# Optimization experiments

Measured on AMD Instinct MI355X. Metric: run time of the kernel, lower is better.

## Reference

```python
import jax, jax.numpy as jnp
import numpy as np

B, L, E, H = 2, 2048, 1024, 16
D = E // H  # 64


def setup_inputs() -> dict:
    key = jax.random.key(0)
    ks = jax.random.split(key, 9)
    return {
        "query": jax.random.normal(ks[0], (B, L, E), dtype=jnp.float32),
        "value": jax.random.normal(ks[1], (B, L, E), dtype=jnp.float32),
        "key": jax.random.normal(ks[2], (B, L, E), dtype=jnp.float32),
        "mask": jax.random.randint(ks[3], (B, 1, L, L), 0, 2, dtype=jnp.int32),
        "Wq": jax.random.normal(ks[4], (D, D), dtype=jnp.float32) * 0.05,
        "Wk": jax.random.normal(ks[5], (D, D), dtype=jnp.float32) * 0.05,
        "Wv": jax.random.normal(ks[6], (D, D), dtype=jnp.float32) * 0.05,
        "Wfc": jax.random.normal(ks[7], (E, E), dtype=jnp.float32) * 0.02,
        "bfc": jax.random.normal(ks[8], (E,), dtype=jnp.float32) * 0.02,
    }


def reference(query, value, key, mask, Wq, Wk, Wv, Wfc, bfc):
    b, q_len, _ = query.shape
    k_len = key.shape[1]
    v_len = value.shape[1]
    # split heads: [b, l, H, D]
    q = query.reshape(b, q_len, H, D)
    k = key.reshape(b, k_len, H, D)
    v = value.reshape(b, v_len, H, D)
    # per-head linear projections (shared weights across heads, no bias)
    q = jnp.einsum('bqhd,ed->bqhe', q, Wq)
    k = jnp.einsum('bkhd,ed->bkhe', k, Wk)
    v = jnp.einsum('bvhd,ed->bvhe', v, Wv)
    # attention scores [b, H, q, k]
    attn = jnp.einsum('bqhd,bkhd->bhqk', q, k)
    # NOTE: original masks BEFORE scaling, and scales by sqrt(embedding_size)
    attn = jnp.where(mask == 0, jnp.float32(-1e20), attn)
    attn = attn / jnp.float32(E ** 0.5)
    attn = jax.nn.softmax(attn, axis=3)
    out = jnp.einsum('bhqk,bkhd->bqhd', attn, v).reshape(b, q_len, E)
    out = out @ Wfc.T + bfc
    return out
```

## Files before the change

kernel.cpp:

```cpp
#include <hip/hip_runtime.h>
#include <hip/hip_bf16.h>


#define B_ 2
#define L_ 2048
#define E_ 1024
#define H_ 16
#define D_ 64

typedef __attribute__((ext_vector_type(8))) short s8v;
typedef __attribute__((ext_vector_type(4))) float f4v;
typedef __attribute__((ext_vector_type(2))) float f2v;

__device__ __forceinline__ f4v mfma16(s8v a, s8v b, f4v c) {
    return __builtin_amdgcn_mfma_f32_16x16x32_bf16(a, b, c, 0, 0, 0);
}

__device__ __forceinline__ float fast_exp2(float x) {
    return __builtin_amdgcn_exp2f(x);
}

__device__ __forceinline__ ushort bf16bits(float f) {
    __hip_bfloat16 h = __float2bfloat16(f);
    return *(ushort*)&h;
}

__device__ __forceinline__ void glds16(const __hip_bfloat16* g, ushort* l) {
    __builtin_amdgcn_global_load_lds(
        (const __attribute__((address_space(1))) void*)g,
        (__attribute__((address_space(3))) void*)l,
        16, 0, 0);
}

__device__ __forceinline__ s8v ld8_dual(const void* p, size_t idx, bool isf32) {
    if (isf32) {
        const float* pf = (const float*)p + idx;
        f4v f0 = *(const f4v*)pf;
        f4v f1 = *(const f4v*)(pf + 4);
        s8v r;
        r[0] = (short)bf16bits(f0[0]); r[1] = (short)bf16bits(f0[1]);
        r[2] = (short)bf16bits(f0[2]); r[3] = (short)bf16bits(f0[3]);
        r[4] = (short)bf16bits(f1[0]); r[5] = (short)bf16bits(f1[1]);
        r[6] = (short)bf16bits(f1[2]); r[7] = (short)bf16bits(f1[3]);
        return r;
    }
    return *(const s8v*)((const __hip_bfloat16*)p + idx);
}

__device__ __forceinline__ s8v ld8_ws(const __hip_bfloat16* p) {
    return *(const s8v*)p;
}

__device__ __forceinline__ s8v u4_to_s8(uint a, uint b, uint c, uint d) {
    union { uint u[4]; s8v v; } x;
    x.u[0] = a; x.u[1] = b; x.u[2] = c; x.u[3] = d;
    return x.v;
}

__device__ __forceinline__ bool block_detect_f32(const void* q_in, int* sflag) {
    if (threadIdx.x == 0) *sflag = 0;
    __syncthreads();
    const ushort* qq = (const ushort*)q_in + (threadIdx.x & 255) * 16;
    int bad = 0;
    #pragma unroll
    for (int i = 0; i < 16; ++i) bad += (((qq[i] >> 7) & 0xFF) >= 0x8E);
    bad += __shfl_xor(bad, 1);
    bad += __shfl_xor(bad, 2);
    bad += __shfl_xor(bad, 4);
    bad += __shfl_xor(bad, 8);
    bad += __shfl_xor(bad, 16);
    bad += __shfl_xor(bad, 32);
    if ((threadIdx.x & 63) == 0 && threadIdx.x < 256) atomicAdd(sflag, bad);
    __syncthreads();
    return *sflag > 100;
}

__device__ __forceinline__ void cvt_piece(
    size_t i4, const void* Wfc, const void* bfc,
    __hip_bfloat16* wfc_bf, __hip_bfloat16* bfc_bf, bool isf32)
{
    const size_t base = i4 * 4;
    const size_t n1 = (size_t)E_ * E_;
    if (base >= n1 + E_) return;
    const void* src = (base < n1) ? Wfc : bfc;
    const size_t off = (base < n1) ? base : base - n1;
    __hip_bfloat16* dst = (base < n1) ? (wfc_bf + off) : (bfc_bf + off);
    if (isf32) {
        f4v v = *(const f4v*)((const float*)src + off);
        #pragma unroll
        for (int j = 0; j < 4; ++j) dst[j] = __float2bfloat16(v[j]);
    } else {
        *(ushort4*)dst = *(const ushort4*)((const ushort*)src + off);
    }
}

__global__ __launch_bounds__(256) void proj_all_kernel(
    const void* __restrict__ q_in, const void* __restrict__ k_in,
    const void* __restrict__ v_in,
    const void* __restrict__ Wq, const void* __restrict__ Wk,
    const void* __restrict__ Wv,
    const void* __restrict__ Wfc, const void* __restrict__ bfc,
    const int* __restrict__ mask, unsigned long long* __restrict__ mbits,
    __hip_bfloat16* __restrict__ qp, __hip_bfloat16* __restrict__ kp,
    __hip_bfloat16* __restrict__ vpT,
    __hip_bfloat16* __restrict__ wfc_bf, __hip_bfloat16* __restrict__ bfc_bf)
{
    __shared__ __align__(16) ushort tile[64][72];
    __shared__ __align__(16) ushort wlds[64 * 72];
    __shared__ int sflag;
    const int wave = threadIdx.x >> 6;
    const int lane = threadIdx.x & 63;
    const int quad = lane >> 4;
    const int l16  = lane & 15;

    if (blockIdx.y == 3) {
        const int lane_ = threadIdx.x & 63;
        const size_t wbase = (size_t)blockIdx.x * 128 + wave * 32;
        #pragma unroll 4
        for (int i = 0; i < 32; ++i) {
            const size_t widx = wbase + i;
            const int v = mask[widx * 64 + lane_];
            const unsigned long long bal = __ballot(v != 0);
            if (lane_ == 0) mbits[widx] = bal;
        }
        return;
    }

    const bool isf32 = block_detect_f32(q_in, &sflag);

    if (blockIdx.y == 4) {
        cvt_piece((size_t)blockIdx.x * 256 + threadIdx.x, Wfc, bfc, wfc_bf, bfc_bf, isf32);
        if (blockIdx.x == 0)
            cvt_piece((size_t)(E_ * (size_t)E_ / 4) + threadIdx.x, Wfc, bfc, wfc_bf, bfc_bf, isf32);
        return;
    }

    {
        const void* W = blockIdx.y == 0 ? Wq : (blockIdx.y == 1 ? Wk : Wv);
        const int row = threadIdx.x >> 2;
        const int c0  = (threadIdx.x & 3) * 16;
        if (isf32) {
            const float* wsrc = (const float*)W + row * 64 + c0;
            #pragma unroll
            for (int j = 0; j < 16; ++j)
                wlds[row * 72 + c0 + j] = bf16bits(wsrc[j]);
        } else {
            const ushort* wsrc = (const ushort*)W + row * 64 + c0;
            *(s8v*)&wlds[row * 72 + c0]     = *(const s8v*)wsrc;
            *(s8v*)&wlds[row * 72 + c0 + 8] = *(const s8v*)(wsrc + 8);
        }
    }
    __syncthreads();

    if (blockIdx.y < 2) {
        const void* X = blockIdx.y == 0 ? q_in : k_in;
        __hip_bfloat16* dst = blockIdx.y == 0 ? qp : kp;
        const float oscale = (blockIdx.y == 0) ? 0.045084439755930314f : 1.0f;
        const int m0 = (blockIdx.x * 4 + wave) * 16;

        const size_t abase = (size_t)(m0 + l16) * D_;
        s8v a0 = ld8_dual(X, abase + quad * 8, isf32);
        s8v a1 = ld8_dual(X, abase + 32 + quad * 8, isf32);

        f4v acc[4];
        #pragma unroll
        for (int nt = 0; nt < 4; ++nt) {
            const ushort* wr = &wlds[(nt * 16 + l16) * 72];
            s8v b0 = *(const s8v*)(wr + quad * 8);
            s8v b1 = *(const s8v*)(wr + 32 + quad * 8);
            f4v c = {0.f, 0.f, 0.f, 0.f};
            c = mfma16(a0, b0, c);
            c = mfma16(a1, b1, c);
            acc[nt] = c;
        }
        #pragma unroll
        for (int r = 0; r < 4; ++r) {
            const int m = m0 + quad * 4 + r;
            const int h = m & 15;
            const int bl = m >> 4;
            const int b = bl >> 11;
            const int l = bl & (L_ - 1);
            #pragma unroll
            for (int nt = 0; nt < 4; ++nt) {
                const int e = nt * 16 + l16;
                dst[(((size_t)(b * H_ + h)) * L_ + l) * D_ + e] =
                    __float2bfloat16(acc[nt][r] * oscale);
            }
        }
    } else {
        const int l0 = (blockIdx.x & 31) * 64;
        const int bh = blockIdx.x >> 5;
        const int b = bh >> 4, h = bh & 15;
        const int lw = l0 + wave * 16;

        const size_t xbase = ((size_t)(b * L_ + lw + l16)) * E_ + h * D_;
        s8v a0 = ld8_dual(v_in, xbase + quad * 8, isf32);
        s8v a1 = ld8_dual(v_in, xbase + 32 + quad * 8, isf32);

        #pragma unroll
        for (int nt = 0; nt < 4; ++nt) {
            const int e = nt * 16 + l16;
            const ushort* wr = &wlds[e * 72];
            s8v b0 = *(const s8v*)(wr + quad * 8);
            s8v b1 = *(const s8v*)(wr + 32 + quad * 8);
            f4v c = {0.f, 0.f, 0.f, 0.f};
            c = mfma16(a0, b0, c);
            c = mfma16(a1, b1, c);
            #pragma unroll
            for (int r = 0; r < 4; ++r)
                tile[wave * 16 + quad * 4 + r][e] = bf16bits(c[r]);
        }
        __syncthreads();
        const int e  = threadIdx.x >> 2;
        const int lc = (threadIdx.x & 3) * 16;
        s8v s0, s1;
        #pragma unroll
        for (int i = 0; i < 8; ++i) {
            s0[i] = (short)tile[lc + i][e];
            s1[i] = (short)tile[lc + 8 + i][e];
        }
        __hip_bfloat16* drow = vpT + ((size_t)bh * D_ + e) * L_ + l0 + lc;
        *(s8v*)drow = s0;
        *(s8v*)(drow + 8) = s1;
    }
}

__global__ __launch_bounds__(256) void cvt_wfc_kernel(
    const void* __restrict__ Wfc, const void* __restrict__ bfc,
    __hip_bfloat16* __restrict__ wfc_bf, __hip_bfloat16* __restrict__ bfc_bf,
    const void* __restrict__ q_in)
{
    __shared__ int sflag;
    const bool isf32 = block_detect_f32(q_in, &sflag);
    cvt_piece((size_t)blockIdx.x * 256 + threadIdx.x, Wfc, bfc, wfc_bf, bfc_bf, isf32);
}

__global__ __launch_bounds__(512, 2) void attn_kernel(
    const __hip_bfloat16* __restrict__ qp,
    const __hip_bfloat16* __restrict__ kp,
    const __hip_bfloat16* __restrict__ vpT,
    const unsigned long long* __restrict__ mbits,
    __hip_bfloat16* __restrict__ attn_out)
{
    __shared__ __align__(16) ushort kv[4][2][64 * 64];

    const int wave = threadIdx.x >> 6;
    const int lane = threadIdx.x & 63;
    const int quad = lane >> 4;
    const int l16  = lane & 15;
    const int sw   = l16 & 7;
    const int bh = blockIdx.y;
    const int b = bh >> 4, h = bh & 15;
    const int q0 = blockIdx.x * 128 + wave * 16;

    const __hip_bfloat16* kbh = kp + (size_t)bh * L_ * D_;
    const __hip_bfloat16* vbh = vpT + (size_t)bh * D_ * L_;
    const unsigned long long* mrow = mbits + ((size_t)b * L_ + q0 + l16) * 32;

    const int lrow = lane >> 3;
    const int lchk = (lane & 7) ^ lrow;
    const int r0 = wave * 8;
    const __hip_bfloat16* kg = kbh + (size_t)(r0 + lrow) * D_ + lchk * 8;
    const __hip_bfloat16* vg = vbh + (size_t)(r0 + lrow) * L_ + lchk * 8;

    const __hip_bfloat16* qbase = qp + ((size_t)bh * L_ + q0) * D_;
    s8v qa0 = ld8_ws(qbase + (size_t)l16 * D_ + quad * 8);
    s8v qa1 = ld8_ws(qbase + (size_t)l16 * D_ + 32 + quad * 8);

    f2v rs2 = {0.f, 0.f};
    f4v o[4];
    #pragma unroll
    for (int nt = 0; nt < 4; ++nt) o[nt] = (f4v){0.f, 0.f, 0.f, 0.f};

    const int ro0 = l16 * 64 + ((quad ^ sw) << 3);
    const int ro1 = l16 * 64 + (((quad + 4) ^ sw) << 3);
    const int shq = quad * 4;

    unsigned long long wq0 = 0, wq1 = 0, wq2 = 0, wq3 = 0;

    glds16(kg, &kv[0][0][r0 * 64]);
    glds16(vg, &kv[0][1][r0 * 64]);
    wq0 = mrow[0];
    kg += 64 * D_; vg += 64;
    glds16(kg, &kv[1][0][r0 * 64]);
    glds16(vg, &kv[1][1][r0 * 64]);
    wq1 = mrow[1];
    kg += 64 * D_; vg += 64;

#define ATTN_BODY(IT_, CUR_, DST_, PRE_, VMASM_)                               \
    {                                                                          \
        if (PRE_) {                                                            \
            glds16(kg, &kv[DST_][0][r0 * 64]);                                 \
            glds16(vg, &kv[DST_][1][r0 * 64]);                                 \
            wq##DST_ = mrow[(IT_) + 2];                                        \
            kg += 64 * D_; vg += 64;                                           \
        }                                                                      \
        asm volatile(VMASM_ ::: "memory");                                     \
        __builtin_amdgcn_s_barrier();                                          \
        __builtin_amdgcn_sched_barrier(0);                                     \
        const uint wlo_sh = ((uint)wq##CUR_) >> shq;                           \
        const uint whi_sh = ((uint)(wq##CUR_ >> 32)) >> shq;                   \
        f4v s_[4];                                                             \
        __builtin_amdgcn_s_setprio(1);                                         \
        _Pragma("unroll")                                                      \
        for (int nt = 0; nt < 4; ++nt) {                                       \
            s8v kb0 = *(const s8v*)&kv[CUR_][0][nt * 1024 + ro0];              \
            s8v kb1 = *(const s8v*)&kv[CUR_][0][nt * 1024 + ro1];              \
            f4v c = {0.f, 0.f, 0.f, 0.f};                                      \
            c = mfma16(kb0, qa0, c);                                           \
            c = mfma16(kb1, qa1, c);                                           \
            s_[nt] = c;                                                        \
        }                                                                      \
        __builtin_amdgcn_s_setprio(0);                                         \
        uint dw[4][2];                                                         \
        _Pragma("unroll")                                                      \
        for (int nt = 0; nt < 4; ++nt) {                                       \
            const uint hs = (nt & 2) ? whi_sh : wlo_sh;                        \
            float pr[4];                                                       \
            _Pragma("unroll")                                                  \
            for (int r = 0; r < 4; ++r) {                                      \
                const float p = fast_exp2(s_[nt][r]);                          \
                const int m = __builtin_amdgcn_sbfe((int)hs,                   \
                                  ((nt & 1) << 4) + r, 1);                     \
                pr[r] = __uint_as_float(__float_as_uint(p) & (uint)m);         \
            }                                                                  \
            rs2 += (f2v){pr[0], pr[1]};                                        \
            rs2 += (f2v){pr[2], pr[3]};                                        \
            asm("v_cvt_pk_bf16_f32 %0, %1, %2"                                 \
                : "=v"(dw[nt][0]) : "v"(pr[0]), "v"(pr[1]));                   \
            asm("v_cvt_pk_bf16_f32 %0, %1, %2"                                 \
                : "=v"(dw[nt][1]) : "v"(pr[2]), "v"(pr[3]));                   \
        }                                                                      \
        uint w00 = dw[0][0], w10 = dw[1][0];                                   \
        uint w01 = dw[0][1], w11 = dw[1][1];                                   \
        uint w20 = dw[2][0], w30 = dw[3][0];                                   \
        uint w21 = dw[2][1], w31 = dw[3][1];                                   \
        asm("v_permlane32_swap_b32 %0, %1" : "+v"(w00), "+v"(w10));            \
        asm("v_permlane16_swap_b32 %0, %1" : "+v"(w00), "+v"(w10));            \
        asm("v_permlane32_swap_b32 %0, %1" : "+v"(w01), "+v"(w11));            \
        asm("v_permlane16_swap_b32 %0, %1" : "+v"(w01), "+v"(w11));            \
        asm("v_permlane32_swap_b32 %0, %1" : "+v"(w20), "+v"(w30));            \
        asm("v_permlane16_swap_b32 %0, %1" : "+v"(w20), "+v"(w30));            \
        asm("v_permlane32_swap_b32 %0, %1" : "+v"(w21), "+v"(w31));            \
        asm("v_permlane16_swap_b32 %0, %1" : "+v"(w21), "+v"(w31));            \
        s8v pa0 = u4_to_s8(w00, w01, w10, w11);                                \
        s8v pa1 = u4_to_s8(w20, w21, w30, w31);                                \
        __builtin_amdgcn_s_setprio(1);                                         \
        _Pragma("unroll")                                                      \
        for (int nt = 0; nt < 4; ++nt) {                                       \
            s8v vb0 = *(const s8v*)&kv[CUR_][1][nt * 1024 + ro0];              \
            s8v vb1 = *(const s8v*)&kv[CUR_][1][nt * 1024 + ro1];              \
            o[nt] = mfma16(pa0, vb0, o[nt]);                                   \
            o[nt] = mfma16(pa1, vb1, o[nt]);                                   \
        }                                                                      \
        __builtin_amdgcn_s_setprio(0);                                         \
    }

    for (int it4 = 0; it4 < 7; ++it4) {
        const int t = it4 * 4;
        ATTN_BODY(t,     0, 2, true, "s_waitcnt vmcnt(6)")
        ATTN_BODY(t + 1, 1, 3, true, "s_waitcnt vmcnt(6)")
        ATTN_BODY(t + 2, 2, 0, true, "s_waitcnt vmcnt(6)")
        ATTN_BODY(t + 3, 3, 1, true, "s_waitcnt vmcnt(6)")
    }
    ATTN_BODY(28, 0, 2, true,  "s_waitcnt vmcnt(6)")
    ATTN_BODY(29, 1, 3, true,  "s_waitcnt vmcnt(6)")
    ATTN_BODY(30, 2, 0, false, "s_waitcnt vmcnt(3)")
    ATTN_BODY(31, 3, 1, false, "s_waitcnt vmcnt(0)")
#undef ATTN_BODY

    float v = rs2[0] + rs2[1];
    v += __shfl_xor(v, 16, 64);
    v += __shfl_xor(v, 32, 64);
    #pragma unroll
    for (int r = 0; r < 4; ++r) {
        const int qrow = quad * 4 + r;
        const float li = __shfl(v, qrow, 64);
        const float inv = 1.0f / fmaxf(li, 1e-30f);
        const int row = q0 + qrow;
        #pragma unroll
        for (int nt = 0; nt < 4; ++nt) {
            const int d = nt * 16 + l16;
            attn_out[((size_t)(b * L_ + row)) * E_ + h * D_ + d] =
                __float2bfloat16(o[nt][r] * inv);
        }
    }
}

__global__ __launch_bounds__(256, 4) void fc_kernel(
    const __hip_bfloat16* __restrict__ x,
    const __hip_bfloat16* __restrict__ wfc_bf,
    const __hip_bfloat16* __restrict__ bfc_bf,
    void* __restrict__ out, const void* __restrict__ q_in)
{
    __shared__ __align__(16) ushort abuf[2][128 * 64];
    __shared__ __align__(16) ushort bbuf[2][64 * 64];
    __shared__ int sflag;
    const bool isf32 = block_detect_f32(q_in, &sflag);
    const int wave = threadIdx.x >> 6;
    const int lane = threadIdx.x & 63;
    const int quad = lane >> 4;
    const int l16  = lane & 15;
    const int sw   = l16 & 7;
    const int m0 = blockIdx.x * 128;
    const int n0 = blockIdx.y * 64;
    const int wr = wave >> 1;
    const int wc = wave & 1;

    const int lrow = lane >> 3;
    const int lchk = (lane & 7) ^ lrow;

    const __hip_bfloat16* ag[4];
    #pragma unroll
    for (int c = 0; c < 4; ++c)
        ag[c] = x + (size_t)(m0 + c * 32 + wave * 8 + lrow) * E_ + lchk * 8;
    const __hip_bfloat16* bg[2];
    #pragma unroll
    for (int c = 0; c < 2; ++c)
        bg[c] = wfc_bf + (size_t)(n0 + c * 32 + wave * 8 + lrow) * E_ + lchk * 8;

    f4v acc[4][2];
    #pragma unroll
    for (int fm = 0; fm < 4; ++fm)
        #pragma unroll
        for (int fn = 0; fn < 2; ++fn) acc[fm][fn] = (f4v){0.f, 0.f, 0.f, 0.f};

    #pragma unroll
    for (int c = 0; c < 4; ++c) glds16(ag[c], &abuf[0][(c * 32 + wave * 8) * 64]);
    #pragma unroll
    for (int c = 0; c < 2; ++c) glds16(bg[c], &bbuf[0][(c * 32 + wave * 8) * 64]);
    __syncthreads();

    int cur = 0;
    for (int it = 0; it < 16; ++it) {
        if (it < 15) {
            #pragma unroll
            for (int c = 0; c < 4; ++c)
                glds16(ag[c] + (it + 1) * 64, &abuf[cur ^ 1][(c * 32 + wave * 8) * 64]);
            #pragma unroll
            for (int c = 0; c < 2; ++c)
                glds16(bg[c] + (it + 1) * 64, &bbuf[cur ^ 1][(c * 32 + wave * 8) * 64]);
        }
        s8v a0[4], a1[4];
        #pragma unroll
        for (int fm = 0; fm < 4; ++fm) {
            const ushort* ar = &abuf[cur][(wr * 64 + fm * 16 + l16) * 64];
            a0[fm] = *(const s8v*)(ar + ((quad ^ sw) << 3));
            a1[fm] = *(const s8v*)(ar + (((quad + 4) ^ sw) << 3));
        }
        #pragma unroll
        for (int fn = 0; fn < 2; ++fn) {
            const ushort* br = &bbuf[cur][(wc * 32 + fn * 16 + l16) * 64];
            s8v b0 = *(const s8v*)(br + ((quad ^ sw) << 3));
            s8v b1 = *(const s8v*)(br + (((quad + 4) ^ sw) << 3));
            #pragma unroll
            for (int fm = 0; fm < 4; ++fm) {
                acc[fm][fn] = mfma16(a0[fm], b0, acc[fm][fn]);
                acc[fm][fn] = mfma16(a1[fm], b1, acc[fm][fn]);
            }
        }
        __syncthreads();
        cur ^= 1;
    }
    #pragma unroll
    for (int fm = 0; fm < 4; ++fm) {
        #pragma unroll
        for (int r = 0; r < 4; ++r) {
            const int m = m0 + wr * 64 + fm * 16 + quad * 4 + r;
            #pragma unroll
            for (int fn = 0; fn < 2; ++fn) {
                const int n = n0 + wc * 32 + fn * 16 + l16;
                const float val = acc[fm][fn][r] + __bfloat162float(bfc_bf[n]);
                if (isf32) ((float*)out)[(size_t)m * E_ + n] = val;
                else       ((__hip_bfloat16*)out)[(size_t)m * E_ + n] = __float2bfloat16(val);
            }
        }
    }
}

extern "C" void kernel_launch(void* const* d_in, const int* in_sizes, int n_in,
                              void* d_out, int out_size, void* d_ws, size_t ws_size,
                              hipStream_t stream) {
    const void* query = d_in[0];
    const void* value = d_in[1];
    const void* key   = d_in[2];
    const int*  mask  = (const int*)d_in[3];
    const void* Wq  = d_in[4];
    const void* Wk  = d_in[5];
    const void* Wv  = d_in[6];
    const void* Wfc = d_in[7];
    const void* bfc = d_in[8];

    char* ws = (char*)d_ws;
    unsigned long long* mbits     = (unsigned long long*)(ws + (64u << 10));
    __hip_bfloat16* qp            = (__hip_bfloat16*)(ws + (2u  << 20));
    __hip_bfloat16* kp            = (__hip_bfloat16*)(ws + (10u << 20));
    __hip_bfloat16* vpT           = (__hip_bfloat16*)(ws + (18u << 20));
    __hip_bfloat16* attn_out      = (__hip_bfloat16*)(ws + (26u << 20));

    const bool big_ws = ws_size >= (37ull << 20);
    __hip_bfloat16* wfc_bf = big_ws ? (__hip_bfloat16*)(ws + (34ull << 20)) : qp;
    __hip_bfloat16* bfc_bf = wfc_bf + (size_t)E_ * E_;

    proj_all_kernel<<<dim3(1024, big_ws ? 5 : 4), 256, 0, stream>>>(
        query, key, value, Wq, Wk, Wv, Wfc, bfc, mask, mbits,
        qp, kp, vpT, wfc_bf, bfc_bf);
    attn_kernel<<<dim3(16, 32), 512, 0, stream>>>(qp, kp, vpT, mbits, attn_out);
    if (!big_ws)
        cvt_wfc_kernel<<<1025, 256, 0, stream>>>(Wfc, bfc, wfc_bf, bfc_bf, query);
    fc_kernel<<<dim3(32, 16), 256, 0, stream>>>(attn_out, wfc_bf, bfc_bf, d_out, query);
}
```

Measured before the change: 214.2 us.

## Give each attention wave two 16-row query tiles, halving block size

The attention kernel now runs 4 waves of 256 threads per block instead of 8 waves of 512, and each wave handles 32 query rows as two 16-row sub-tiles. Each K/V fragment read from LDS is reused for both sub-tiles, which halves LDS read traffic per MFMA and doubles the K/V staging work per thread. The trade-off is more accumulator and score registers per wave and fewer waves to hide latency, which may lower occupancy.

```diff
diff --git a/kernel.cpp b/kernel.cpp
--- a/kernel.cpp
+++ b/kernel.cpp
@@ -235,7 +235,7 @@
     cvt_piece((size_t)blockIdx.x * 256 + threadIdx.x, Wfc, bfc, wfc_bf, bfc_bf, isf32);
 }
 
-__global__ __launch_bounds__(512, 2) void attn_kernel(
+__global__ __launch_bounds__(256, 2) void attn_kernel(
     const __hip_bfloat16* __restrict__ qp,
     const __hip_bfloat16* __restrict__ kp,
     const __hip_bfloat16* __restrict__ vpT,
@@ -251,81 +251,71 @@
     const int sw   = l16 & 7;
     const int bh = blockIdx.y;
     const int b = bh >> 4, h = bh & 15;
-    const int q0 = blockIdx.x * 128 + wave * 16;
+    const int q0 = blockIdx.x * 128 + wave * 32;
 
     const __hip_bfloat16* kbh = kp + (size_t)bh * L_ * D_;
     const __hip_bfloat16* vbh = vpT + (size_t)bh * D_ * L_;
-    const unsigned long long* mrow = mbits + ((size_t)b * L_ + q0 + l16) * 32;
+    const unsigned long long* mrowA = mbits + ((size_t)b * L_ + q0 + l16) * 32;
+    const unsigned long long* mrowB = mrowA + 16 * 32;
 
     const int lrow = lane >> 3;
     const int lchk = (lane & 7) ^ lrow;
-    const int r0 = wave * 8;
-    const __hip_bfloat16* kg = kbh + (size_t)(r0 + lrow) * D_ + lchk * 8;
-    const __hip_bfloat16* vg = vbh + (size_t)(r0 + lrow) * L_ + lchk * 8;
+    const int r0 = wave * 16;
+    const __hip_bfloat16* kg0 = kbh + (size_t)(r0 + lrow) * D_ + lchk * 8;
+    const __hip_bfloat16* kg1 = kbh + (size_t)(r0 + 8 + lrow) * D_ + lchk * 8;
+    const __hip_bfloat16* vg0 = vbh + (size_t)(r0 + lrow) * L_ + lchk * 8;
+    const __hip_bfloat16* vg1 = vbh + (size_t)(r0 + 8 + lrow) * L_ + lchk * 8;
 
     const __hip_bfloat16* qbase = qp + ((size_t)bh * L_ + q0) * D_;
-    s8v qa0 = ld8_ws(qbase + (size_t)l16 * D_ + quad * 8);
-    s8v qa1 = ld8_ws(qbase + (size_t)l16 * D_ + 32 + quad * 8);
-
-    f2v rs2 = {0.f, 0.f};
-    f4v o[4];
-    #pragma unroll
-    for (int nt = 0; nt < 4; ++nt) o[nt] = (f4v){0.f, 0.f, 0.f, 0.f};
+    s8v qaA0 = ld8_ws(qbase + (size_t)l16 * D_ + quad * 8);
+    s8v qaA1 = ld8_ws(qbase + (size_t)l16 * D_ + 32 + quad * 8);
+    s8v qaB0 = ld8_ws(qbase + (size_t)(16 + l16) * D_ + quad * 8);
+    s8v qaB1 = ld8_ws(qbase + (size_t)(16 + l16) * D_ + 32 + quad * 8);
+
+    f2v rs2A = {0.f, 0.f}, rs2B = {0.f, 0.f};
+    f4v oA[4], oB[4];
+    #pragma unroll
+    for (int nt = 0; nt < 4; ++nt) {
+        oA[nt] = (f4v){0.f, 0.f, 0.f, 0.f};
+        oB[nt] = (f4v){0.f, 0.f, 0.f, 0.f};
+    }
 
     const int ro0 = l16 * 64 + ((quad ^ sw) << 3);
     const int ro1 = l16 * 64 + (((quad + 4) ^ sw) << 3);
     const int shq = quad * 4;
 
-    unsigned long long wq0 = 0, wq1 = 0, wq2 = 0, wq3 = 0;
-
-    glds16(kg, &kv[0][0][r0 * 64]);
-    glds16(vg, &kv[0][1][r0 * 64]);
-    wq0 = mrow[0];
-    kg += 64 * D_; vg += 64;
-    glds16(kg, &kv[1][0][r0 * 64]);
-    glds16(vg, &kv[1][1][r0 * 64]);
-    wq1 = mrow[1];
-    kg += 64 * D_; vg += 64;
-
-#define ATTN_BODY(IT_, CUR_, DST_, PRE_, VMASM_)                               \
+    unsigned long long wqA0 = 0, wqA1 = 0, wqA2 = 0, wqA3 = 0;
+    unsigned long long wqB0 = 0, wqB1 = 0, wqB2 = 0, wqB3 = 0;
+
+    glds16(kg0, &kv[0][0][r0 * 64]);
+    glds16(kg1, &kv[0][0][r0 * 64 + 512]);
+    glds16(vg0, &kv[0][1][r0 * 64]);
+    glds16(vg1, &kv[0][1][r0 * 64 + 512]);
+    wqA0 = mrowA[0]; wqB0 = mrowB[0];
+    kg0 += 64 * D_; kg1 += 64 * D_; vg0 += 64; vg1 += 64;
+    glds16(kg0, &kv[1][0][r0 * 64]);
+    glds16(kg1, &kv[1][0][r0 * 64 + 512]);
+    glds16(vg0, &kv[1][1][r0 * 64]);
+    glds16(vg1, &kv[1][1][r0 * 64 + 512]);
+    wqA1 = mrowA[1]; wqB1 = mrowB[1];
+    kg0 += 64 * D_; kg1 += 64 * D_; vg0 += 64; vg1 += 64;
+
+#define SM_T(SARR_, WLO_, WHI_, RS_, PA0_, PA1_)                               \
     {                                                                          \
-        if (PRE_) {                                                            \
-            glds16(kg, &kv[DST_][0][r0 * 64]);                                 \
-            glds16(vg, &kv[DST_][1][r0 * 64]);                                 \
-            wq##DST_ = mrow[(IT_) + 2];                                        \
-            kg += 64 * D_; vg += 64;                                           \
-        }                                                                      \
-        asm volatile(VMASM_ ::: "memory");                                     \
-        __builtin_amdgcn_s_barrier();                                          \
-        __builtin_amdgcn_sched_barrier(0);                                     \
-        const uint wlo_sh = ((uint)wq##CUR_) >> shq;                           \
-        const uint whi_sh = ((uint)(wq##CUR_ >> 32)) >> shq;                   \
-        f4v s_[4];                                                             \
-        __builtin_amdgcn_s_setprio(1);                                         \
-        _Pragma("unroll")                                                      \
-        for (int nt = 0; nt < 4; ++nt) {                                       \
-            s8v kb0 = *(const s8v*)&kv[CUR_][0][nt * 1024 + ro0];              \
-            s8v kb1 = *(const s8v*)&kv[CUR_][0][nt * 1024 + ro1];              \
-            f4v c = {0.f, 0.f, 0.f, 0.f};                                      \
-            c = mfma16(kb0, qa0, c);                                           \
-            c = mfma16(kb1, qa1, c);                                           \
-            s_[nt] = c;                                                        \
-        }                                                                      \
-        __builtin_amdgcn_s_setprio(0);                                         \
         uint dw[4][2];                                                         \
         _Pragma("unroll")                                                      \
         for (int nt = 0; nt < 4; ++nt) {                                       \
-            const uint hs = (nt & 2) ? whi_sh : wlo_sh;                        \
+            const uint hs = (nt & 2) ? WHI_ : WLO_;                            \
             float pr[4];                                                       \
             _Pragma("unroll")                                                  \
             for (int r = 0; r < 4; ++r) {                                      \
-                const float p = fast_exp2(s_[nt][r]);                          \
+                const float p = fast_exp2(SARR_[nt][r]);                       \
                 const int m = __builtin_amdgcn_sbfe((int)hs,                   \
                                   ((nt & 1) << 4) + r, 1);                     \
                 pr[r] = __uint_as_float(__float_as_uint(p) & (uint)m);         \
             }                                                                  \
-            rs2 += (f2v){pr[0], pr[1]};                                        \
-            rs2 += (f2v){pr[2], pr[3]};                                        \
+            RS_ += (f2v){pr[0], pr[1]};                                        \
+            RS_ += (f2v){pr[2], pr[3]};                                        \
             asm("v_cvt_pk_bf16_f32 %0, %1, %2"                                 \
                 : "=v"(dw[nt][0]) : "v"(pr[0]), "v"(pr[1]));                   \
             asm("v_cvt_pk_bf16_f32 %0, %1, %2"                                 \
@@ -343,46 +333,95 @@
         asm("v_permlane16_swap_b32 %0, %1" : "+v"(w20), "+v"(w30));            \
         asm("v_permlane32_swap_b32 %0, %1" : "+v"(w21), "+v"(w31));            \
         asm("v_permlane16_swap_b32 %0, %1" : "+v"(w21), "+v"(w31));            \
-        s8v pa0 = u4_to_s8(w00, w01, w10, w11);                                \
-        s8v pa1 = u4_to_s8(w20, w21, w30, w31);                                \
+        PA0_ = u4_to_s8(w00, w01, w10, w11);                                   \
+        PA1_ = u4_to_s8(w20, w21, w30, w31);                                   \
+    }
+
+#define ATTN_BODY(IT_, CUR_, DST_, PRE_, VMASM_)                               \
+    {                                                                          \
+        if (PRE_) {                                                            \
+            glds16(kg0, &kv[DST_][0][r0 * 64]);                                \
+            glds16(kg1, &kv[DST_][0][r0 * 64 + 512]);                          \
+            glds16(vg0, &kv[DST_][1][r0 * 64]);                                \
+            glds16(vg1, &kv[DST_][1][r0 * 64 + 512]);                          \
+            wqA##DST_ = mrowA[(IT_) + 2];                                      \
+            wqB##DST_ = mrowB[(IT_) + 2];                                      \
+            kg0 += 64 * D_; kg1 += 64 * D_; vg0 += 64; vg1 += 64;              \
+        }                                                                      \
+        asm volatile(VMASM_ ::: "memory");                                     \
+        __builtin_amdgcn_s_barrier();                                          \
+        __builtin_amdgcn_sched_barrier(0);                                     \
+        const uint wloA = ((uint)wqA##CUR_) >> shq;                            \
+        const uint whiA = ((uint)(wqA##CUR_ >> 32)) >> shq;                    \
+        const uint wloB = ((uint)wqB##CUR_) >> shq;                            \
+        const uint whiB = ((uint)(wqB##CUR_ >> 32)) >> shq;                    \
+        f4v sA[4], sB[4];                                                      \
+        __builtin_amdgcn_s_setprio(1);                                         \
+        _Pragma("unroll")                                                      \
+        for (int nt = 0; nt < 4; ++nt) {                                       \
+            s8v kb0 = *(const s8v*)&kv[CUR_][0][nt * 1024 + ro0];              \
+            s8v kb1 = *(const s8v*)&kv[CUR_][0][nt * 1024 + ro1];              \
+            f4v cA = {0.f, 0.f, 0.f, 0.f};                                     \
+            f4v cB = {0.f, 0.f, 0.f, 0.f};                                     \
+            cA = mfma16(kb0, qaA0, cA);                                        \
+            cA = mfma16(kb1, qaA1, cA);                                        \
+            cB = mfma16(kb0, qaB0, cB);                                        \
+            cB = mfma16(kb1, qaB1, cB);                                        \
+            sA[nt] = cA; sB[nt] = cB;                                          \
+        }                                                                      \
+        __builtin_amdgcn_s_setprio(0);                                         \
+        s8v paA0, paA1, paB0, paB1;                                            \
+        SM_T(sA, wloA, whiA, rs2A, paA0, paA1)                                 \
+        SM_T(sB, wloB, whiB, rs2B, paB0, paB1)                                 \
         __builtin_amdgcn_s_setprio(1);                                         \
         _Pragma("unroll")                                                      \
         for (int nt = 0; nt < 4; ++nt) {                                       \
             s8v vb0 = *(const s8v*)&kv[CUR_][1][nt * 1024 + ro0];              \
             s8v vb1 = *(const s8v*)&kv[CUR_][1][nt * 1024 + ro1];              \
-            o[nt] = mfma16(pa0, vb0, o[nt]);                                   \
-            o[nt] = mfma16(pa1, vb1, o[nt]);                                   \
+            oA[nt] = mfma16(paA0, vb0, oA[nt]);                                \
+            oA[nt] = mfma16(paA1, vb1, oA[nt]);                                \
+            oB[nt] = mfma16(paB0, vb0, oB[nt]);                                \
+            oB[nt] = mfma16(paB1, vb1, oB[nt]);                                \
         }                                                                      \
         __builtin_amdgcn_s_setprio(0);                                         \
     }
 
     for (int it4 = 0; it4 < 7; ++it4) {
         const int t = it4 * 4;
-        ATTN_BODY(t,     0, 2, true, "s_waitcnt vmcnt(6)")
-        ATTN_BODY(t + 1, 1, 3, true, "s_waitcnt vmcnt(6)")
-        ATTN_BODY(t + 2, 2, 0, true, "s_waitcnt vmcnt(6)")
-        ATTN_BODY(t + 3, 3, 1, true, "s_waitcnt vmcnt(6)")
-    }
-    ATTN_BODY(28, 0, 2, true,  "s_waitcnt vmcnt(6)")
-    ATTN_BODY(29, 1, 3, true,  "s_waitcnt vmcnt(6)")
-    ATTN_BODY(30, 2, 0, false, "s_waitcnt vmcnt(3)")
+        ATTN_BODY(t,     0, 2, true, "s_waitcnt vmcnt(12)")
+        ATTN_BODY(t + 1, 1, 3, true, "s_waitcnt vmcnt(12)")
+        ATTN_BODY(t + 2, 2, 0, true, "s_waitcnt vmcnt(12)")
+        ATTN_BODY(t + 3, 3, 1, true, "s_waitcnt vmcnt(12)")
+    }
+    ATTN_BODY(28, 0, 2, true,  "s_waitcnt vmcnt(12)")
+    ATTN_BODY(29, 1, 3, true,  "s_waitcnt vmcnt(12)")
+    ATTN_BODY(30, 2, 0, false, "s_waitcnt vmcnt(6)")
     ATTN_BODY(31, 3, 1, false, "s_waitcnt vmcnt(0)")
 #undef ATTN_BODY
-
-    float v = rs2[0] + rs2[1];
-    v += __shfl_xor(v, 16, 64);
-    v += __shfl_xor(v, 32, 64);
+#undef SM_T
+
+    float vA = rs2A[0] + rs2A[1];
+    vA += __shfl_xor(vA, 16, 64);
+    vA += __shfl_xor(vA, 32, 64);
+    float vB = rs2B[0] + rs2B[1];
+    vB += __shfl_xor(vB, 16, 64);
+    vB += __shfl_xor(vB, 32, 64);
     #pragma unroll
     for (int r = 0; r < 4; ++r) {
         const int qrow = quad * 4 + r;
-        const float li = __shfl(v, qrow, 64);
-        const float inv = 1.0f / fmaxf(li, 1e-30f);
-        const int row = q0 + qrow;
+        const float liA = __shfl(vA, qrow, 64);
+        const float invA = 1.0f / fmaxf(liA, 1e-30f);
+        const float liB = __shfl(vB, qrow, 64);
+        const float invB = 1.0f / fmaxf(liB, 1e-30f);
+        const int rowA = q0 + qrow;
+        const int rowB = q0 + 16 + qrow;
         #pragma unroll
         for (int nt = 0; nt < 4; ++nt) {
             const int d = nt * 16 + l16;
-            attn_out[((size_t)(b * L_ + row)) * E_ + h * D_ + d] =
-                __float2bfloat16(o[nt][r] * inv);
+            attn_out[((size_t)(b * L_ + rowA)) * E_ + h * D_ + d] =
+                __float2bfloat16(oA[nt][r] * invA);
+            attn_out[((size_t)(b * L_ + rowB)) * E_ + h * D_ + d] =
+                __float2bfloat16(oB[nt][r] * invB);
         }
     }
 }
@@ -505,7 +544,7 @@
     proj_all_kernel<<<dim3(1024, big_ws ? 5 : 4), 256, 0, stream>>>(
         query, key, value, Wq, Wk, Wv, Wfc, bfc, mask, mbits,
         qp, kp, vpT, wfc_bf, bfc_bf);
-    attn_kernel<<<dim3(16, 32), 512, 0, stream>>>(qp, kp, vpT, mbits, attn_out);
+    attn_kernel<<<dim3(16, 32), 256, 0, stream>>>(qp, kp, vpT, mbits, attn_out);
     if (!big_ws)
         cvt_wfc_kernel<<<1025, 256, 0, stream>>>(Wfc, bfc, wfc_bf, bfc_bf, query);
     fc_kernel<<<dim3(32, 16), 256, 0, stream>>>(attn_out, wfc_bf, bfc_bf, d_out, query);
```

Measured after the change: 221.0 us. 1.03x slower.

## Fuse Wfc fp32-to-bf16 conversion into the FC GEMM's B-tile load

Applied to the files above, without the earlier changes.

Drops the separate Wfc/bias conversion pass, done either as extra blocks in the projection kernel or as a standalone kernel. The FC kernel now reads fp32 Wfc directly into registers, converts it with packed bf16 conversion instructions, and writes the result into the LDS double buffer after the MFMA work, so the load overlaps compute. This removes a full write and re-read of the bf16 weight copy and possibly a kernel launch. The cost is that each of the 32 M-blocks re-reads fp32 weights (twice the bytes of bf16) through registers instead of async global-to-LDS loads, which adds VGPR pressure.

```diff
diff --git a/kernel.cpp b/kernel.cpp
--- a/kernel.cpp
+++ b/kernel.cpp
@@ -57,6 +57,15 @@
     return x.v;
 }
 
+__device__ __forceinline__ void store_cvt8(ushort* dst, f4v a, f4v b) {
+    uint d0, d1, d2, d3;
+    asm("v_cvt_pk_bf16_f32 %0, %1, %2" : "=v"(d0) : "v"(a[0]), "v"(a[1]));
+    asm("v_cvt_pk_bf16_f32 %0, %1, %2" : "=v"(d1) : "v"(a[2]), "v"(a[3]));
+    asm("v_cvt_pk_bf16_f32 %0, %1, %2" : "=v"(d2) : "v"(b[0]), "v"(b[1]));
+    asm("v_cvt_pk_bf16_f32 %0, %1, %2" : "=v"(d3) : "v"(b[2]), "v"(b[3]));
+    *(s8v*)dst = u4_to_s8(d0, d1, d2, d3);
+}
+
 __device__ __forceinline__ bool block_detect_f32(const void* q_in, int* sflag) {
     if (threadIdx.x == 0) *sflag = 0;
     __syncthreads();
@@ -75,35 +84,14 @@
     return *sflag > 100;
 }
 
-__device__ __forceinline__ void cvt_piece(
-    size_t i4, const void* Wfc, const void* bfc,
-    __hip_bfloat16* wfc_bf, __hip_bfloat16* bfc_bf, bool isf32)
-{
-    const size_t base = i4 * 4;
-    const size_t n1 = (size_t)E_ * E_;
-    if (base >= n1 + E_) return;
-    const void* src = (base < n1) ? Wfc : bfc;
-    const size_t off = (base < n1) ? base : base - n1;
-    __hip_bfloat16* dst = (base < n1) ? (wfc_bf + off) : (bfc_bf + off);
-    if (isf32) {
-        f4v v = *(const f4v*)((const float*)src + off);
-        #pragma unroll
-        for (int j = 0; j < 4; ++j) dst[j] = __float2bfloat16(v[j]);
-    } else {
-        *(ushort4*)dst = *(const ushort4*)((const ushort*)src + off);
-    }
-}
-
 __global__ __launch_bounds__(256) void proj_all_kernel(
     const void* __restrict__ q_in, const void* __restrict__ k_in,
     const void* __restrict__ v_in,
     const void* __restrict__ Wq, const void* __restrict__ Wk,
     const void* __restrict__ Wv,
-    const void* __restrict__ Wfc, const void* __restrict__ bfc,
     const int* __restrict__ mask, unsigned long long* __restrict__ mbits,
     __hip_bfloat16* __restrict__ qp, __hip_bfloat16* __restrict__ kp,
-    __hip_bfloat16* __restrict__ vpT,
-    __hip_bfloat16* __restrict__ wfc_bf, __hip_bfloat16* __restrict__ bfc_bf)
+    __hip_bfloat16* __restrict__ vpT)
 {
     __shared__ __align__(16) ushort tile[64][72];
     __shared__ __align__(16) ushort wlds[64 * 72];
@@ -128,13 +116,6 @@
 
     const bool isf32 = block_detect_f32(q_in, &sflag);
 
-    if (blockIdx.y == 4) {
-        cvt_piece((size_t)blockIdx.x * 256 + threadIdx.x, Wfc, bfc, wfc_bf, bfc_bf, isf32);
-        if (blockIdx.x == 0)
-            cvt_piece((size_t)(E_ * (size_t)E_ / 4) + threadIdx.x, Wfc, bfc, wfc_bf, bfc_bf, isf32);
-        return;
-    }
-
     {
         const void* W = blockIdx.y == 0 ? Wq : (blockIdx.y == 1 ? Wk : Wv);
         const int row = threadIdx.x >> 2;
@@ -223,16 +204,6 @@
         *(s8v*)drow = s0;
         *(s8v*)(drow + 8) = s1;
     }
-}
-
-__global__ __launch_bounds__(256) void cvt_wfc_kernel(
-    const void* __restrict__ Wfc, const void* __restrict__ bfc,
-    __hip_bfloat16* __restrict__ wfc_bf, __hip_bfloat16* __restrict__ bfc_bf,
-    const void* __restrict__ q_in)
-{
-    __shared__ int sflag;
-    const bool isf32 = block_detect_f32(q_in, &sflag);
-    cvt_piece((size_t)blockIdx.x * 256 + threadIdx.x, Wfc, bfc, wfc_bf, bfc_bf, isf32);
 }
 
 __global__ __launch_bounds__(512, 2) void attn_kernel(
@@ -389,8 +360,8 @@
 
 __global__ __launch_bounds__(256, 4) void fc_kernel(
     const __hip_bfloat16* __restrict__ x,
-    const __hip_bfloat16* __restrict__ wfc_bf,
-    const __hip_bfloat16* __restrict__ bfc_bf,
+    const void* __restrict__ Wfc,
+    const void* __restrict__ bfc,
     void* __restrict__ out, const void* __restrict__ q_in)
 {
     __shared__ __align__(16) ushort abuf[2][128 * 64];
@@ -414,10 +385,14 @@
     #pragma unroll
     for (int c = 0; c < 4; ++c)
         ag[c] = x + (size_t)(m0 + c * 32 + wave * 8 + lrow) * E_ + lchk * 8;
-    const __hip_bfloat16* bg[2];
-    #pragma unroll
-    for (int c = 0; c < 2; ++c)
-        bg[c] = wfc_bf + (size_t)(n0 + c * 32 + wave * 8 + lrow) * E_ + lchk * 8;
+    const __hip_bfloat16* bgh[2];
+    const float* bgf[2];
+    #pragma unroll
+    for (int c = 0; c < 2; ++c) {
+        const size_t roff = (size_t)(n0 + c * 32 + wave * 8 + lrow) * E_ + lchk * 8;
+        bgh[c] = (const __hip_bfloat16*)Wfc + roff;
+        bgf[c] = (const float*)Wfc + roff;
+    }
 
     f4v acc[4][2];
     #pragma unroll
@@ -427,19 +402,37 @@
 
     #pragma unroll
     for (int c = 0; c < 4; ++c) glds16(ag[c], &abuf[0][(c * 32 + wave * 8) * 64]);
-    #pragma unroll
-    for (int c = 0; c < 2; ++c) glds16(bg[c], &bbuf[0][(c * 32 + wave * 8) * 64]);
+    if (!isf32) {
+        #pragma unroll
+        for (int c = 0; c < 2; ++c) glds16(bgh[c], &bbuf[0][(c * 32 + wave * 8) * 64]);
+    } else {
+        #pragma unroll
+        for (int c = 0; c < 2; ++c) {
+            f4v u0 = *(const f4v*)bgf[c];
+            f4v u1 = *(const f4v*)(bgf[c] + 4);
+            store_cvt8(&bbuf[0][(c * 32 + wave * 8) * 64 + lane * 8], u0, u1);
+        }
+    }
     __syncthreads();
 
     int cur = 0;
     for (int it = 0; it < 16; ++it) {
+        f4v pw0[2], pw1[2];
         if (it < 15) {
             #pragma unroll
             for (int c = 0; c < 4; ++c)
                 glds16(ag[c] + (it + 1) * 64, &abuf[cur ^ 1][(c * 32 + wave * 8) * 64]);
-            #pragma unroll
-            for (int c = 0; c < 2; ++c)
-                glds16(bg[c] + (it + 1) * 64, &bbuf[cur ^ 1][(c * 32 + wave * 8) * 64]);
+            if (!isf32) {
+                #pragma unroll
+                for (int c = 0; c < 2; ++c)
+                    glds16(bgh[c] + (it + 1) * 64, &bbuf[cur ^ 1][(c * 32 + wave * 8) * 64]);
+            } else {
+                #pragma unroll
+                for (int c = 0; c < 2; ++c) {
+                    pw0[c] = *(const f4v*)(bgf[c] + (it + 1) * 64);
+                    pw1[c] = *(const f4v*)(bgf[c] + (it + 1) * 64 + 4);
+                }
+            }
         }
         s8v a0[4], a1[4];
         #pragma unroll
@@ -459,6 +452,12 @@
                 acc[fm][fn] = mfma16(a1[fm], b1, acc[fm][fn]);
             }
         }
+        if (it < 15 && isf32) {
+            #pragma unroll
+            for (int c = 0; c < 2; ++c)
+                store_cvt8(&bbuf[cur ^ 1][(c * 32 + wave * 8) * 64 + lane * 8],
+                           pw0[c], pw1[c]);
+        }
         __syncthreads();
         cur ^= 1;
     }
@@ -470,7 +469,10 @@
             #pragma unroll
             for (int fn = 0; fn < 2; ++fn) {
                 const int n = n0 + wc * 32 + fn * 16 + l16;
-                const float val = acc[fm][fn][r] + __bfloat162float(bfc_bf[n]);
+                const float bias = isf32
+                    ? ((const float*)bfc)[n]
+                    : __bfloat162float(((const __hip_bfloat16*)bfc)[n]);
+                const float val = acc[fm][fn][r] + bias;
                 if (isf32) ((float*)out)[(size_t)m * E_ + n] = val;
                 else       ((__hip_bfloat16*)out)[(size_t)m * E_ + n] = __float2bfloat16(val);
             }
@@ -498,15 +500,8 @@
     __hip_bfloat16* vpT           = (__hip_bfloat16*)(ws + (18u << 20));
     __hip_bfloat16* attn_out      = (__hip_bfloat16*)(ws + (26u << 20));
 
-    const bool big_ws = ws_size >= (37ull << 20);
-    __hip_bfloat16* wfc_bf = big_ws ? (__hip_bfloat16*)(ws + (34ull << 20)) : qp;
-    __hip_bfloat16* bfc_bf = wfc_bf + (size_t)E_ * E_;
-
-    proj_all_kernel<<<dim3(1024, big_ws ? 5 : 4), 256, 0, stream>>>(
-        query, key, value, Wq, Wk, Wv, Wfc, bfc, mask, mbits,
-        qp, kp, vpT, wfc_bf, bfc_bf);
+    proj_all_kernel<<<dim3(1024, 4), 256, 0, stream>>>(
+        query, key, value, Wq, Wk, Wv, mask, mbits, qp, kp, vpT);
     attn_kernel<<<dim3(16, 32), 512, 0, stream>>>(qp, kp, vpT, mbits, attn_out);
-    if (!big_ws)
-        cvt_wfc_kernel<<<1025, 256, 0, stream>>>(Wfc, bfc, wfc_bf, bfc_bf, query);
-    fc_kernel<<<dim3(32, 16), 256, 0, stream>>>(attn_out, wfc_bf, bfc_bf, d_out, query);
-}
+    fc_kernel<<<dim3(32, 16), 256, 0, stream>>>(attn_out, Wfc, bfc, d_out, query);
+}
```

Result: slower. 225.4 us (+5.2%).
